# Kernel tuning notes

Hardware: AMD Instinct MI355X
Metric: run time of the kernel (lower is better)

The kernel has to match this reference:

```python
import jax, jax.numpy as jnp
import numpy as np

EPS = 1e-4


def setup_inputs() -> dict:
    key = jax.random.key(0)
    ks = jax.random.split(key, 16)
    N, D, H, K = 262144, 162, 256, 30
    s = 0.05  # weight init scale
    return {
        "Yh": jax.random.uniform(ks[0], (N, D), dtype=jnp.float32),
        "u": jax.random.uniform(ks[1], (1,), dtype=jnp.float32),
        "W1": jax.random.normal(ks[2], (D, H), dtype=jnp.float32) * s,
        "b1": jnp.zeros((H,), jnp.float32),
        "W2": jax.random.normal(ks[3], (H, H), dtype=jnp.float32) * s,
        "b2": jnp.zeros((H,), jnp.float32),
        "Wa": jax.random.normal(ks[4], (H, K), dtype=jnp.float32) * s,
        "ba": jnp.zeros((K,), jnp.float32),
        "Wb": jax.random.normal(ks[5], (H, K), dtype=jnp.float32) * s,
        "bb": jnp.zeros((K,), jnp.float32),
        "Wd1": jax.random.normal(ks[6], (K, H), dtype=jnp.float32) * s,
        "bd1": jnp.zeros((H,), jnp.float32),
        "Wd2": jax.random.normal(ks[7], (H, D), dtype=jnp.float32) * s,
        "bd2": jnp.zeros((D,), jnp.float32),
    }


def _stick_segments(v):
    # pi_k = v_k * prod_{j<k} (1 - v_j)  (vectorized exclusive cumprod,
    # replacing the original per-dim Python loop)
    cp = jnp.cumprod(1.0 - v, axis=1)  # [N, K]
    excl = jnp.concatenate([jnp.ones_like(v[:, :1]), cp[:, :-1]], axis=1)
    return v * excl


def reference(Yh, u, W1, b1, W2, b2, Wa, ba, Wb, bb, Wd1, bd1, Wd2, bd2):
    # encode_hsi: dense MLP -> positive Kumaraswamy params (softplus heads)
    h = jax.nn.relu(Yh @ W1 + b1)
    h = jax.nn.relu(h @ W2 + b2)
    alpha = jax.nn.softplus(h @ Wa + ba) + EPS  # param1_hsi [N, K]
    beta = jax.nn.softplus(h @ Wb + bb) + EPS   # param2_hsi [N, K]
    # Kumaraswamy reparametrization with a single shared uniform sample
    uu = u[0] * 0.98 + 0.01  # Uniform(0.01, 0.99) scalar
    v = (1.0 - uu ** (1.0 / beta)) ** (1.0 / alpha)  # [N, K]
    # set_v_K_to_one: force last stick proportion to 1
    v = jnp.concatenate([v[:, :-1], jnp.ones_like(v[:, :1])], axis=1)
    pi_h = _stick_segments(v)  # [N, K], rows sum to 1
    # decode: MLP -> sigmoid (positive outputs, recon.log() finite)
    d = jax.nn.relu(pi_h @ Wd1 + bd1)
    recon = jax.nn.sigmoid(d @ Wd2 + bd2)  # [N, D]
    return recon, alpha, beta, pi_h
```

## Files before the change

kernel.cpp:

```cpp
#include <hip/hip_runtime.h>
#include <hip/hip_bf16.h>

#define N_ROWS 262144
#define D_IN 162
#define H_DIM 256
#define K_DIM 30

using bf16_t = __hip_bfloat16;
typedef __attribute__((ext_vector_type(8))) short bf16x8;
typedef __attribute__((ext_vector_type(4))) float f32x4;

__device__ __forceinline__ int swz_idx(int row, int col) {
  int byte = (row << 9) + (col << 1);
  byte ^= (row & 7) << 4;
  return byte >> 1;
}

__device__ __forceinline__ float softplus_f(float x) {
  return (x > 15.f) ? x : log1pf(__expf(x));
}

__global__ void pack_b_kernel(const float* __restrict__ src, bf16_t* __restrict__ dst,
                              int K, int N, int Np, int KB) {
  int idx = blockIdx.x * 256 + threadIdx.x;
  int total = KB * Np * 32;
  if (idx >= total) return;
  int ks = idx & 31;
  int n  = (idx >> 5) % Np;
  int kb = idx / (32 * Np);
  int k  = kb * 32 + ks;
  float v = (k < K && n < N) ? src[k * N + n] : 0.f;
  dst[idx] = __float2bfloat16(v);
}

__global__ void pack_ab_kernel(const float* __restrict__ Wa, const float* __restrict__ Wb,
                               bf16_t* __restrict__ dst) {
  int idx = blockIdx.x * 256 + threadIdx.x;
  if (idx >= 8 * 64 * 32) return;
  int ks = idx & 31;
  int n  = (idx >> 5) & 63;
  int kb = idx >> 11;
  int k  = kb * 32 + ks;
  float v = 0.f;
  if (n < 30)                 v = Wa[k * 30 + n];
  else if (n >= 32 && n < 62) v = Wb[k * 30 + (n - 32)];
  dst[idx] = __float2bfloat16(v);
}

template<int KB, int NP>
__device__ __forceinline__ void gemm_tile(const bf16_t* __restrict__ A,
                                          const bf16_t* __restrict__ Bp,
                                          int colBase, int lr, int lg,
                                          f32x4 acc[4][4]) {
#pragma unroll
  for (int kb = 0; kb < KB; ++kb) {
    bf16x8 a[4], b[4];
#pragma unroll
    for (int m = 0; m < 4; ++m)
      a[m] = *reinterpret_cast<const bf16x8*>(A + swz_idx(16 * m + lr, kb * 32 + 8 * lg));
#pragma unroll
    for (int n = 0; n < 4; ++n)
      b[n] = *reinterpret_cast<const bf16x8*>(Bp + ((kb * NP + colBase + 16 * n + lr) << 5) + 8 * lg);
#pragma unroll
    for (int m = 0; m < 4; ++m)
#pragma unroll
      for (int n = 0; n < 4; ++n)
        acc[m][n] = __builtin_amdgcn_mfma_f32_16x16x32_bf16(a[m], b[n], acc[m][n], 0, 0, 0);
  }
}

__device__ __forceinline__ void epilogue_relu(f32x4 acc[4][4], const float* __restrict__ bias,
                                              bf16_t* __restrict__ Out, int colBase,
                                              int lr, int lg) {
#pragma unroll
  for (int n = 0; n < 4; ++n) {
    int col = colBase + 16 * n + lr;
    float bv = bias[col];
#pragma unroll
    for (int m = 0; m < 4; ++m)
#pragma unroll
      for (int i = 0; i < 4; ++i) {
        float x = acc[m][n][i] + bv;
        x = fmaxf(x, 0.f);
        Out[swz_idx(16 * m + 4 * lg + i, col)] = __float2bfloat16(x);
      }
  }
}

__launch_bounds__(256, 2)
__global__ void usdn_fused(const float* __restrict__ Yh, const float* __restrict__ u,
                           const float* __restrict__ b1, const float* __restrict__ b2,
                           const float* __restrict__ ba, const float* __restrict__ bb,
                           const float* __restrict__ bd1, const float* __restrict__ bd2,
                           const bf16_t* __restrict__ Wp1, const bf16_t* __restrict__ Wp2,
                           const bf16_t* __restrict__ Wpab, const bf16_t* __restrict__ Wpd1,
                           const bf16_t* __restrict__ Wpd2,
                           float* __restrict__ outRecon, float* __restrict__ outAlpha,
                           float* __restrict__ outBeta, float* __restrict__ outPi) {
  __shared__ bf16_t bufA[64 * 256];
  __shared__ bf16_t bufB[64 * 256];

  const int tid = threadIdx.x;
  const int w  = tid >> 6;
  const int l  = tid & 63;
  const int lr = l & 15;
  const int lg = l >> 4;
  const int r0 = blockIdx.x << 6;

  {
    const float4* src = reinterpret_cast<const float4*>(Yh + (size_t)r0 * D_IN);
    for (int i = tid; i < (64 * D_IN) / 4; i += 256) {
      float4 f = src[i];
      int base = i << 2;
#pragma unroll
      for (int e = 0; e < 4; ++e) {
        int idx = base + e;
        int row = idx / D_IN;
        int col = idx - row * D_IN;
        bufA[swz_idx(row, col)] = __float2bfloat16((&f.x)[e]);
      }
    }
    for (int i = tid; i < 64 * (192 - D_IN); i += 256) {
      int row = i / 30;
      int col = D_IN + (i - row * 30);
      bufA[swz_idx(row, col)] = __float2bfloat16(0.f);
    }
  }
  __syncthreads();

  {
    f32x4 acc[4][4] = {};
    gemm_tile<6, 256>(bufA, Wp1, w * 64, lr, lg, acc);
    epilogue_relu(acc, b1, bufB, w * 64, lr, lg);
  }
  __syncthreads();

  {
    f32x4 acc[4][4] = {};
    gemm_tile<8, 256>(bufB, Wp2, w * 64, lr, lg, acc);
    epilogue_relu(acc, b2, bufA, w * 64, lr, lg);
  }
  __syncthreads();

  {
    f32x4 acc3[4] = {};
#pragma unroll
    for (int kb = 0; kb < 8; ++kb) {
      bf16x8 a = *reinterpret_cast<const bf16x8*>(bufA + swz_idx(16 * w + lr, kb * 32 + 8 * lg));
#pragma unroll
      for (int n = 0; n < 4; ++n) {
        bf16x8 b = *reinterpret_cast<const bf16x8*>(Wpab + ((kb * 64 + 16 * n + lr) << 5) + 8 * lg);
        acc3[n] = __builtin_amdgcn_mfma_f32_16x16x32_bf16(a, b, acc3[n], 0, 0, 0);
      }
    }
    float uu  = u[0] * 0.98f + 0.01f;
    float l2u = log2f(uu);
    float* vbuf = reinterpret_cast<float*>(bufB);
#pragma unroll
    for (int n = 0; n < 2; ++n) {
      int j = 16 * n + lr;
      bool valid = (j < K_DIM);
      float bva = valid ? ba[j] : 0.f;
      float bvb = valid ? bb[j] : 0.f;
#pragma unroll
      for (int i = 0; i < 4; ++i) {
        int row = 16 * w + 4 * lg + i;
        if (valid) {
          float alpha = softplus_f(acc3[n][i] + bva) + 1e-4f;
          float beta  = softplus_f(acc3[n + 2][i] + bvb) + 1e-4f;
          size_t gro = (size_t)(r0 + row);
          outAlpha[gro * K_DIM + j] = alpha;
          outBeta [gro * K_DIM + j] = beta;
          float v;
          if (j == K_DIM - 1) v = 1.f;
          else {
            float t = exp2f(l2u / beta);
            v = exp2f(log2f(1.f - t) / alpha);
          }
          vbuf[row * 33 + j] = v;
        }
      }
    }
  }
  __syncthreads();

  if (tid < 64) {
    const float* vbuf = reinterpret_cast<const float*>(bufB);
    int row = tid;
    size_t gro = (size_t)(r0 + row);
    float ex = 1.f;
#pragma unroll
    for (int j = 0; j < K_DIM - 1; ++j) {
      float vj = vbuf[row * 33 + j];
      float pi = vj * ex;
      outPi[gro * K_DIM + j] = pi;
      bufA[row * 40 + j] = __float2bfloat16(pi);
      ex *= (1.f - vj);
    }
    outPi[gro * K_DIM + (K_DIM - 1)] = ex;
    bufA[row * 40 + 29] = __float2bfloat16(ex);
    bufA[row * 40 + 30] = __float2bfloat16(0.f);
    bufA[row * 40 + 31] = __float2bfloat16(0.f);
  }
  __syncthreads();

  {
    f32x4 acc[4][4] = {};
    bf16x8 a[4];
#pragma unroll
    for (int m = 0; m < 4; ++m)
      a[m] = *reinterpret_cast<const bf16x8*>(bufA + (16 * m + lr) * 40 + 8 * lg);
#pragma unroll
    for (int n = 0; n < 4; ++n) {
      bf16x8 b = *reinterpret_cast<const bf16x8*>(Wpd1 + ((w * 64 + 16 * n + lr) << 5) + 8 * lg);
#pragma unroll
      for (int m = 0; m < 4; ++m)
        acc[m][n] = __builtin_amdgcn_mfma_f32_16x16x32_bf16(a[m], b, acc[m][n], 0, 0, 0);
    }
    epilogue_relu(acc, bd1, bufB, w * 64, lr, lg);
  }
  __syncthreads();

  {
    f32x4 acc[4][3] = {};
#pragma unroll
    for (int kb = 0; kb < 8; ++kb) {
      bf16x8 a[4];
#pragma unroll
      for (int m = 0; m < 4; ++m)
        a[m] = *reinterpret_cast<const bf16x8*>(bufB + swz_idx(16 * m + lr, kb * 32 + 8 * lg));
#pragma unroll
      for (int n = 0; n < 3; ++n) {
        bf16x8 b = *reinterpret_cast<const bf16x8*>(Wpd2 + ((kb * 192 + w * 48 + 16 * n + lr) << 5) + 8 * lg);
#pragma unroll
        for (int m = 0; m < 4; ++m)
          acc[m][n] = __builtin_amdgcn_mfma_f32_16x16x32_bf16(a[m], b, acc[m][n], 0, 0, 0);
      }
    }
#pragma unroll
    for (int n = 0; n < 3; ++n) {
      int col = w * 48 + 16 * n + lr;
      if (col < D_IN) {
        float bv = bd2[col];
#pragma unroll
        for (int m = 0; m < 4; ++m)
#pragma unroll
          for (int i = 0; i < 4; ++i) {
            int row = 16 * m + 4 * lg + i;
            float x = acc[m][n][i] + bv;
            float s = 1.f / (1.f + __expf(-x));
            outRecon[(size_t)(r0 + row) * D_IN + col] = s;
          }
      }
    }
  }
}

extern "C" void kernel_launch(void* const* d_in, const int* in_sizes, int n_in,
                              void* d_out, int out_size, void* d_ws, size_t ws_size,
                              hipStream_t stream) {
  const float* Yh  = (const float*)d_in[0];
  const float* u   = (const float*)d_in[1];
  const float* W1  = (const float*)d_in[2];
  const float* b1  = (const float*)d_in[3];
  const float* W2  = (const float*)d_in[4];
  const float* b2  = (const float*)d_in[5];
  const float* Wa  = (const float*)d_in[6];
  const float* ba  = (const float*)d_in[7];
  const float* Wb  = (const float*)d_in[8];
  const float* bb  = (const float*)d_in[9];
  const float* Wd1 = (const float*)d_in[10];
  const float* bd1 = (const float*)d_in[11];
  const float* Wd2 = (const float*)d_in[12];
  const float* bd2 = (const float*)d_in[13];

  bf16_t* ws   = (bf16_t*)d_ws;
  bf16_t* Wp1  = ws;
  bf16_t* Wp2  = Wp1 + 49152;
  bf16_t* Wpab = Wp2 + 65536;
  bf16_t* Wpd1 = Wpab + 16384;
  bf16_t* Wpd2 = Wpd1 + 8192;

  float* outRecon = (float*)d_out;
  float* outAlpha = outRecon + (size_t)N_ROWS * D_IN;
  float* outBeta  = outAlpha + (size_t)N_ROWS * K_DIM;
  float* outPi    = outBeta  + (size_t)N_ROWS * K_DIM;

  pack_b_kernel<<<192, 256, 0, stream>>>(W1, Wp1, 162, 256, 256, 6);
  pack_b_kernel<<<256, 256, 0, stream>>>(W2, Wp2, 256, 256, 256, 8);
  pack_ab_kernel<<<64, 256, 0, stream>>>(Wa, Wb, Wpab);
  pack_b_kernel<<<32, 256, 0, stream>>>(Wd1, Wpd1, 30, 256, 256, 1);
  pack_b_kernel<<<192, 256, 0, stream>>>(Wd2, Wpd2, 256, 162, 192, 8);

  usdn_fused<<<N_ROWS / 64, 256, 0, stream>>>(Yh, u, b1, b2, ba, bb, bd1, bd2,
                                              Wp1, Wp2, Wpab, Wpd1, Wpd2,
                                              outRecon, outAlpha, outBeta, outPi);
}
```

Measured before the change: 308.5 us.

## Halve rows per block to 32 and raise occupancy to four blocks per CU

Each block now handles 32 rows instead of 64, which halves the LDS buffers (32 KB total) and the accumulator register tiles, and the launch bound goes from 2 to 4 blocks per CU. The second GEMM writes its output back into the same hidden buffer after an extra barrier, and the pi tile is placed inside the Y buffer, so the block needs only two shared buffers. The goal is more resident waves to hide global-memory and LDS latency. The cost is that every weight fragment is now read from global/L2 once per 32 rows instead of once per 64, which doubles weight traffic, and the alpha/beta stage runs on only two of the four waves.

```diff
diff --git a/kernel.cpp b/kernel.cpp
--- a/kernel.cpp
+++ b/kernel.cpp
@@ -5,6 +5,7 @@
 #define D_IN 162
 #define H_DIM 256
 #define K_DIM 30
+#define ROWS 32
 
 using bf16_t = __hip_bfloat16;
 typedef __attribute__((ext_vector_type(8))) short bf16x8;
@@ -47,47 +48,7 @@
   dst[idx] = __float2bfloat16(v);
 }
 
-template<int KB, int NP>
-__device__ __forceinline__ void gemm_tile(const bf16_t* __restrict__ A,
-                                          const bf16_t* __restrict__ Bp,
-                                          int colBase, int lr, int lg,
-                                          f32x4 acc[4][4]) {
-#pragma unroll
-  for (int kb = 0; kb < KB; ++kb) {
-    bf16x8 a[4], b[4];
-#pragma unroll
-    for (int m = 0; m < 4; ++m)
-      a[m] = *reinterpret_cast<const bf16x8*>(A + swz_idx(16 * m + lr, kb * 32 + 8 * lg));
-#pragma unroll
-    for (int n = 0; n < 4; ++n)
-      b[n] = *reinterpret_cast<const bf16x8*>(Bp + ((kb * NP + colBase + 16 * n + lr) << 5) + 8 * lg);
-#pragma unroll
-    for (int m = 0; m < 4; ++m)
-#pragma unroll
-      for (int n = 0; n < 4; ++n)
-        acc[m][n] = __builtin_amdgcn_mfma_f32_16x16x32_bf16(a[m], b[n], acc[m][n], 0, 0, 0);
-  }
-}
-
-__device__ __forceinline__ void epilogue_relu(f32x4 acc[4][4], const float* __restrict__ bias,
-                                              bf16_t* __restrict__ Out, int colBase,
-                                              int lr, int lg) {
-#pragma unroll
-  for (int n = 0; n < 4; ++n) {
-    int col = colBase + 16 * n + lr;
-    float bv = bias[col];
-#pragma unroll
-    for (int m = 0; m < 4; ++m)
-#pragma unroll
-      for (int i = 0; i < 4; ++i) {
-        float x = acc[m][n][i] + bv;
-        x = fmaxf(x, 0.f);
-        Out[swz_idx(16 * m + 4 * lg + i, col)] = __float2bfloat16(x);
-      }
-  }
-}
-
-__launch_bounds__(256, 2)
+__launch_bounds__(256, 4)
 __global__ void usdn_fused(const float* __restrict__ Yh, const float* __restrict__ u,
                            const float* __restrict__ b1, const float* __restrict__ b2,
                            const float* __restrict__ ba, const float* __restrict__ bb,
@@ -97,56 +58,111 @@
                            const bf16_t* __restrict__ Wpd2,
                            float* __restrict__ outRecon, float* __restrict__ outAlpha,
                            float* __restrict__ outBeta, float* __restrict__ outPi) {
-  __shared__ bf16_t bufA[64 * 256];
-  __shared__ bf16_t bufB[64 * 256];
+  __shared__ bf16_t bufY[ROWS * 256];
+  __shared__ bf16_t bufH[ROWS * 256];
 
   const int tid = threadIdx.x;
   const int w  = tid >> 6;
   const int l  = tid & 63;
   const int lr = l & 15;
   const int lg = l >> 4;
-  const int r0 = blockIdx.x << 6;
+  const int r0 = blockIdx.x * ROWS;
 
   {
     const float4* src = reinterpret_cast<const float4*>(Yh + (size_t)r0 * D_IN);
-    for (int i = tid; i < (64 * D_IN) / 4; i += 256) {
-      float4 f = src[i];
-      int base = i << 2;
-#pragma unroll
-      for (int e = 0; e < 4; ++e) {
-        int idx = base + e;
-        int row = idx / D_IN;
-        int col = idx - row * D_IN;
-        bufA[swz_idx(row, col)] = __float2bfloat16((&f.x)[e]);
-      }
-    }
-    for (int i = tid; i < 64 * (192 - D_IN); i += 256) {
+#pragma unroll
+    for (int it = 0; it < 6; ++it) {
+      int i = tid + it * 256;
+      if (i < (ROWS * D_IN) / 4) {
+        float4 f = src[i];
+        int base = i << 2;
+#pragma unroll
+        for (int e = 0; e < 4; ++e) {
+          int idx = base + e;
+          int row = idx / D_IN;
+          int col = idx - row * D_IN;
+          bufY[swz_idx(row, col)] = __float2bfloat16((&f.x)[e]);
+        }
+      }
+    }
+    for (int i = tid; i < ROWS * 30; i += 256) {
       int row = i / 30;
       int col = D_IN + (i - row * 30);
-      bufA[swz_idx(row, col)] = __float2bfloat16(0.f);
-    }
-  }
-  __syncthreads();
-
-  {
-    f32x4 acc[4][4] = {};
-    gemm_tile<6, 256>(bufA, Wp1, w * 64, lr, lg, acc);
-    epilogue_relu(acc, b1, bufB, w * 64, lr, lg);
-  }
-  __syncthreads();
-
-  {
-    f32x4 acc[4][4] = {};
-    gemm_tile<8, 256>(bufB, Wp2, w * 64, lr, lg, acc);
-    epilogue_relu(acc, b2, bufA, w * 64, lr, lg);
-  }
-  __syncthreads();
-
-  {
+      bufY[swz_idx(row, col)] = __float2bfloat16(0.f);
+    }
+  }
+  __syncthreads();
+
+  {
+    f32x4 acc[2][4] = {};
+#pragma unroll
+    for (int kb = 0; kb < 6; ++kb) {
+      bf16x8 a[2], b[4];
+#pragma unroll
+      for (int m = 0; m < 2; ++m)
+        a[m] = *reinterpret_cast<const bf16x8*>(bufY + swz_idx(16 * m + lr, kb * 32 + 8 * lg));
+#pragma unroll
+      for (int n = 0; n < 4; ++n)
+        b[n] = *reinterpret_cast<const bf16x8*>(Wp1 + ((kb * 256 + w * 64 + 16 * n + lr) << 5) + 8 * lg);
+#pragma unroll
+      for (int m = 0; m < 2; ++m)
+#pragma unroll
+        for (int n = 0; n < 4; ++n)
+          acc[m][n] = __builtin_amdgcn_mfma_f32_16x16x32_bf16(a[m], b[n], acc[m][n], 0, 0, 0);
+    }
+#pragma unroll
+    for (int n = 0; n < 4; ++n) {
+      int col = w * 64 + 16 * n + lr;
+      float bv = b1[col];
+#pragma unroll
+      for (int m = 0; m < 2; ++m)
+#pragma unroll
+        for (int i = 0; i < 4; ++i) {
+          float x = fmaxf(acc[m][n][i] + bv, 0.f);
+          bufH[swz_idx(16 * m + 4 * lg + i, col)] = __float2bfloat16(x);
+        }
+    }
+  }
+  __syncthreads();
+
+  {
+    f32x4 acc[2][4] = {};
+#pragma unroll
+    for (int kb = 0; kb < 8; ++kb) {
+      bf16x8 a[2], b[4];
+#pragma unroll
+      for (int m = 0; m < 2; ++m)
+        a[m] = *reinterpret_cast<const bf16x8*>(bufH + swz_idx(16 * m + lr, kb * 32 + 8 * lg));
+#pragma unroll
+      for (int n = 0; n < 4; ++n)
+        b[n] = *reinterpret_cast<const bf16x8*>(Wp2 + ((kb * 256 + w * 64 + 16 * n + lr) << 5) + 8 * lg);
+#pragma unroll
+      for (int m = 0; m < 2; ++m)
+#pragma unroll
+        for (int n = 0; n < 4; ++n)
+          acc[m][n] = __builtin_amdgcn_mfma_f32_16x16x32_bf16(a[m], b[n], acc[m][n], 0, 0, 0);
+    }
+    __syncthreads();
+#pragma unroll
+    for (int n = 0; n < 4; ++n) {
+      int col = w * 64 + 16 * n + lr;
+      float bv = b2[col];
+#pragma unroll
+      for (int m = 0; m < 2; ++m)
+#pragma unroll
+        for (int i = 0; i < 4; ++i) {
+          float x = fmaxf(acc[m][n][i] + bv, 0.f);
+          bufH[swz_idx(16 * m + 4 * lg + i, col)] = __float2bfloat16(x);
+        }
+    }
+  }
+  __syncthreads();
+
+  if (w < 2) {
     f32x4 acc3[4] = {};
 #pragma unroll
     for (int kb = 0; kb < 8; ++kb) {
-      bf16x8 a = *reinterpret_cast<const bf16x8*>(bufA + swz_idx(16 * w + lr, kb * 32 + 8 * lg));
+      bf16x8 a = *reinterpret_cast<const bf16x8*>(bufH + swz_idx(16 * w + lr, kb * 32 + 8 * lg));
 #pragma unroll
       for (int n = 0; n < 4; ++n) {
         bf16x8 b = *reinterpret_cast<const bf16x8*>(Wpab + ((kb * 64 + 16 * n + lr) << 5) + 8 * lg);
@@ -155,7 +171,7 @@
     }
     float uu  = u[0] * 0.98f + 0.01f;
     float l2u = log2f(uu);
-    float* vbuf = reinterpret_cast<float*>(bufB);
+    float* vbuf = reinterpret_cast<float*>(bufY);
 #pragma unroll
     for (int n = 0; n < 2; ++n) {
       int j = 16 * n + lr;
@@ -184,56 +200,71 @@
   }
   __syncthreads();
 
-  if (tid < 64) {
-    const float* vbuf = reinterpret_cast<const float*>(bufB);
-    int row = tid;
-    size_t gro = (size_t)(r0 + row);
-    float ex = 1.f;
-#pragma unroll
-    for (int j = 0; j < K_DIM - 1; ++j) {
-      float vj = vbuf[row * 33 + j];
-      float pi = vj * ex;
-      outPi[gro * K_DIM + j] = pi;
-      bufA[row * 40 + j] = __float2bfloat16(pi);
-      ex *= (1.f - vj);
-    }
-    outPi[gro * K_DIM + (K_DIM - 1)] = ex;
-    bufA[row * 40 + 29] = __float2bfloat16(ex);
-    bufA[row * 40 + 30] = __float2bfloat16(0.f);
-    bufA[row * 40 + 31] = __float2bfloat16(0.f);
-  }
-  __syncthreads();
-
-  {
-    f32x4 acc[4][4] = {};
-    bf16x8 a[4];
-#pragma unroll
-    for (int m = 0; m < 4; ++m)
-      a[m] = *reinterpret_cast<const bf16x8*>(bufA + (16 * m + lr) * 40 + 8 * lg);
+  {
+    bf16_t* piT = bufY + 4096;
+    if (tid < ROWS) {
+      const float* vbuf = reinterpret_cast<const float*>(bufY);
+      int row = tid;
+      size_t gro = (size_t)(r0 + row);
+      float ex = 1.f;
+#pragma unroll
+      for (int j = 0; j < K_DIM - 1; ++j) {
+        float vj = vbuf[row * 33 + j];
+        float pi = vj * ex;
+        outPi[gro * K_DIM + j] = pi;
+        piT[row * 40 + j] = __float2bfloat16(pi);
+        ex *= (1.f - vj);
+      }
+      outPi[gro * K_DIM + (K_DIM - 1)] = ex;
+      piT[row * 40 + 29] = __float2bfloat16(ex);
+      piT[row * 40 + 30] = __float2bfloat16(0.f);
+      piT[row * 40 + 31] = __float2bfloat16(0.f);
+    }
+  }
+  __syncthreads();
+
+  {
+    const bf16_t* piT = bufY + 4096;
+    f32x4 acc[2][4] = {};
+    bf16x8 a[2];
+#pragma unroll
+    for (int m = 0; m < 2; ++m)
+      a[m] = *reinterpret_cast<const bf16x8*>(piT + (16 * m + lr) * 40 + 8 * lg);
 #pragma unroll
     for (int n = 0; n < 4; ++n) {
       bf16x8 b = *reinterpret_cast<const bf16x8*>(Wpd1 + ((w * 64 + 16 * n + lr) << 5) + 8 * lg);
 #pragma unroll
-      for (int m = 0; m < 4; ++m)
+      for (int m = 0; m < 2; ++m)
         acc[m][n] = __builtin_amdgcn_mfma_f32_16x16x32_bf16(a[m], b, acc[m][n], 0, 0, 0);
     }
-    epilogue_relu(acc, bd1, bufB, w * 64, lr, lg);
-  }
-  __syncthreads();
-
-  {
-    f32x4 acc[4][3] = {};
+#pragma unroll
+    for (int n = 0; n < 4; ++n) {
+      int col = w * 64 + 16 * n + lr;
+      float bv = bd1[col];
+#pragma unroll
+      for (int m = 0; m < 2; ++m)
+#pragma unroll
+        for (int i = 0; i < 4; ++i) {
+          float x = fmaxf(acc[m][n][i] + bv, 0.f);
+          bufH[swz_idx(16 * m + 4 * lg + i, col)] = __float2bfloat16(x);
+        }
+    }
+  }
+  __syncthreads();
+
+  {
+    f32x4 acc[2][3] = {};
 #pragma unroll
     for (int kb = 0; kb < 8; ++kb) {
-      bf16x8 a[4];
-#pragma unroll
-      for (int m = 0; m < 4; ++m)
-        a[m] = *reinterpret_cast<const bf16x8*>(bufB + swz_idx(16 * m + lr, kb * 32 + 8 * lg));
+      bf16x8 a[2];
+#pragma unroll
+      for (int m = 0; m < 2; ++m)
+        a[m] = *reinterpret_cast<const bf16x8*>(bufH + swz_idx(16 * m + lr, kb * 32 + 8 * lg));
 #pragma unroll
       for (int n = 0; n < 3; ++n) {
         bf16x8 b = *reinterpret_cast<const bf16x8*>(Wpd2 + ((kb * 192 + w * 48 + 16 * n + lr) << 5) + 8 * lg);
 #pragma unroll
-        for (int m = 0; m < 4; ++m)
+        for (int m = 0; m < 2; ++m)
           acc[m][n] = __builtin_amdgcn_mfma_f32_16x16x32_bf16(a[m], b, acc[m][n], 0, 0, 0);
       }
     }
@@ -243,7 +274,7 @@
       if (col < D_IN) {
         float bv = bd2[col];
 #pragma unroll
-        for (int m = 0; m < 4; ++m)
+        for (int m = 0; m < 2; ++m)
 #pragma unroll
           for (int i = 0; i < 4; ++i) {
             int row = 16 * m + 4 * lg + i;
@@ -292,7 +323,7 @@
   pack_b_kernel<<<32, 256, 0, stream>>>(Wd1, Wpd1, 30, 256, 256, 1);
   pack_b_kernel<<<192, 256, 0, stream>>>(Wd2, Wpd2, 256, 162, 192, 8);
 
-  usdn_fused<<<N_ROWS / 64, 256, 0, stream>>>(Yh, u, b1, b2, ba, bb, bd1, bd2,
-                                              Wp1, Wp2, Wpab, Wpd1, Wpd2,
-                                              outRecon, outAlpha, outBeta, outPi);
-}
+  usdn_fused<<<N_ROWS / ROWS, 256, 0, stream>>>(Yh, u, b1, b2, ba, bb, bd1, bd2,
+                                                Wp1, Wp2, Wpab, Wpd1, Wpd2,
+                                                outRecon, outAlpha, outBeta, outPi);
+}
```

Measured after the change: 322.2 us. 1.04x slower.

## Halve rows per block, swap MFMA operands, and use a single LDS buffer

Applied to the files above, without the earlier changes.

Each block now handles 32 rows instead of 64, and all stages share one 32 KB LDS buffer, with launch bounds raised to target four blocks per CU. The GEMMs are reformulated with weights as the A operand and activations as B, which transposes the accumulator layout. That allows packed bf16x4 epilogue stores, accumulators seeded with the bias, and interleaved alpha/beta columns. Output stores for recon, alpha, beta and pi are vectorised as float2. Pi is now written out from its bf16-rounded LDS copy, which lowers its precision, and halving the rows per block doubles how often each block reloads the weights.

```diff
diff --git a/kernel.cpp b/kernel.cpp
--- a/kernel.cpp
+++ b/kernel.cpp
@@ -3,19 +3,30 @@
 
 #define N_ROWS 262144
 #define D_IN 162
-#define H_DIM 256
 #define K_DIM 30
+#define ROWS 32
 
 using bf16_t = __hip_bfloat16;
 typedef __attribute__((ext_vector_type(8))) short bf16x8;
 typedef __attribute__((ext_vector_type(4))) float f32x4;
 
-__device__ __forceinline__ int swz_idx(int row, int col) {
-  int byte = (row << 9) + (col << 1);
-  byte ^= (row & 7) << 4;
-  return byte >> 1;
-}
-
+__device__ __forceinline__ int swz_byte(int row, int col) {
+  int b = (row << 9) + (col << 1);
+  return b ^ ((row & 7) << 4);
+}
+
+__device__ __forceinline__ uint32_t bf16b(float x) {
+  return (uint32_t)__builtin_bit_cast(unsigned short, __float2bfloat16(x));
+}
+__device__ __forceinline__ uint32_t pack2(float lo, float hi) {
+  return bf16b(lo) | (bf16b(hi) << 16);
+}
+__device__ __forceinline__ float unpk_lo(uint32_t p) {
+  return __bfloat162float(__builtin_bit_cast(__hip_bfloat16, (unsigned short)(p & 0xffff)));
+}
+__device__ __forceinline__ float unpk_hi(uint32_t p) {
+  return __bfloat162float(__builtin_bit_cast(__hip_bfloat16, (unsigned short)(p >> 16)));
+}
 __device__ __forceinline__ float softplus_f(float x) {
   return (x > 15.f) ? x : log1pf(__expf(x));
 }
@@ -41,53 +52,72 @@
   int n  = (idx >> 5) & 63;
   int kb = idx >> 11;
   int k  = kb * 32 + ks;
-  float v = 0.f;
-  if (n < 30)                 v = Wa[k * 30 + n];
-  else if (n >= 32 && n < 62) v = Wb[k * 30 + (n - 32)];
+  int j = n >> 1, s = n & 1;
+  float v = (j < K_DIM) ? (s ? Wb[k * K_DIM + j] : Wa[k * K_DIM + j]) : 0.f;
   dst[idx] = __float2bfloat16(v);
 }
 
-template<int KB, int NP>
-__device__ __forceinline__ void gemm_tile(const bf16_t* __restrict__ A,
-                                          const bf16_t* __restrict__ Bp,
-                                          int colBase, int lr, int lg,
-                                          f32x4 acc[4][4]) {
+template<int KB, int NP, int NMO>
+__device__ __forceinline__ void gemm_acc(const uint8_t* lds, int srcOff,
+                                         const bf16_t* __restrict__ Wp, int ocBase,
+                                         int lr, int lg, f32x4 (&acc)[NMO][2]) {
+  int bE[2], bO[2];
+#pragma unroll
+  for (int nr = 0; nr < 2; ++nr) {
+    bE[nr] = srcOff + swz_byte(16 * nr + lr, 8 * lg);
+    bO[nr] = srcOff + swz_byte(16 * nr + lr, 32 + 8 * lg);
+  }
 #pragma unroll
   for (int kb = 0; kb < KB; ++kb) {
-    bf16x8 a[4], b[4];
-#pragma unroll
-    for (int m = 0; m < 4; ++m)
-      a[m] = *reinterpret_cast<const bf16x8*>(A + swz_idx(16 * m + lr, kb * 32 + 8 * lg));
-#pragma unroll
-    for (int n = 0; n < 4; ++n)
-      b[n] = *reinterpret_cast<const bf16x8*>(Bp + ((kb * NP + colBase + 16 * n + lr) << 5) + 8 * lg);
-#pragma unroll
-    for (int m = 0; m < 4; ++m)
-#pragma unroll
-      for (int n = 0; n < 4; ++n)
-        acc[m][n] = __builtin_amdgcn_mfma_f32_16x16x32_bf16(a[m], b[n], acc[m][n], 0, 0, 0);
-  }
-}
-
-__device__ __forceinline__ void epilogue_relu(f32x4 acc[4][4], const float* __restrict__ bias,
-                                              bf16_t* __restrict__ Out, int colBase,
-                                              int lr, int lg) {
-#pragma unroll
-  for (int n = 0; n < 4; ++n) {
-    int col = colBase + 16 * n + lr;
-    float bv = bias[col];
-#pragma unroll
-    for (int m = 0; m < 4; ++m)
-#pragma unroll
-      for (int i = 0; i < 4; ++i) {
-        float x = acc[m][n][i] + bv;
-        x = fmaxf(x, 0.f);
-        Out[swz_idx(16 * m + 4 * lg + i, col)] = __float2bfloat16(x);
-      }
-  }
-}
-
-__launch_bounds__(256, 2)
+    bf16x8 wf[NMO];
+#pragma unroll
+    for (int mo = 0; mo < NMO; ++mo)
+      wf[mo] = *reinterpret_cast<const bf16x8*>(Wp + ((kb * NP + ocBase + 16 * mo + lr) << 5) + 8 * lg);
+    bf16x8 hf[2];
+#pragma unroll
+    for (int nr = 0; nr < 2; ++nr) {
+      int base = (kb & 1) ? bO[nr] : bE[nr];
+      hf[nr] = *reinterpret_cast<const bf16x8*>(lds + base + (kb >> 1) * 128);
+    }
+#pragma unroll
+    for (int mo = 0; mo < NMO; ++mo)
+#pragma unroll
+      for (int nr = 0; nr < 2; ++nr)
+        acc[mo][nr] = __builtin_amdgcn_mfma_f32_16x16x32_bf16(wf[mo], hf[nr], acc[mo][nr], 0, 0, 0);
+  }
+}
+
+template<int NMO>
+__device__ __forceinline__ void acc_bias_init(const float* __restrict__ bias, int ocBase,
+                                              int lg, f32x4 (&acc)[NMO][2]) {
+#pragma unroll
+  for (int mo = 0; mo < NMO; ++mo) {
+    float4 bv = *reinterpret_cast<const float4*>(bias + ocBase + 16 * mo + 4 * lg);
+    f32x4 t = {bv.x, bv.y, bv.z, bv.w};
+#pragma unroll
+    for (int nr = 0; nr < 2; ++nr) acc[mo][nr] = t;
+  }
+}
+
+template<int NMO>
+__device__ __forceinline__ void epi_relu_store(uint8_t* lds, int dstOff, int ocBase,
+                                               int lr, int lg, f32x4 (&acc)[NMO][2]) {
+#pragma unroll
+  for (int mo = 0; mo < NMO; ++mo)
+#pragma unroll
+    for (int nr = 0; nr < 2; ++nr) {
+      int row = 16 * nr + lr;
+      int col = ocBase + 16 * mo + 4 * lg;
+      float x0 = fmaxf(acc[mo][nr][0], 0.f), x1 = fmaxf(acc[mo][nr][1], 0.f);
+      float x2 = fmaxf(acc[mo][nr][2], 0.f), x3 = fmaxf(acc[mo][nr][3], 0.f);
+      uint2 p; p.x = pack2(x0, x1); p.y = pack2(x2, x3);
+      *reinterpret_cast<uint2*>(lds + dstOff + swz_byte(row, col)) = p;
+    }
+}
+
+#define OFF_H 16384
+#define OFF_PI 8192
+__launch_bounds__(256, 4)
 __global__ void usdn_fused(const float* __restrict__ Yh, const float* __restrict__ u,
                            const float* __restrict__ b1, const float* __restrict__ b2,
                            const float* __restrict__ ba, const float* __restrict__ bb,
@@ -97,160 +127,164 @@
                            const bf16_t* __restrict__ Wpd2,
                            float* __restrict__ outRecon, float* __restrict__ outAlpha,
                            float* __restrict__ outBeta, float* __restrict__ outPi) {
-  __shared__ bf16_t bufA[64 * 256];
-  __shared__ bf16_t bufB[64 * 256];
+  __shared__ __align__(16) uint8_t lds[32768];
 
   const int tid = threadIdx.x;
   const int w  = tid >> 6;
   const int l  = tid & 63;
   const int lr = l & 15;
   const int lg = l >> 4;
-  const int r0 = blockIdx.x << 6;
-
-  {
-    const float4* src = reinterpret_cast<const float4*>(Yh + (size_t)r0 * D_IN);
-    for (int i = tid; i < (64 * D_IN) / 4; i += 256) {
-      float4 f = src[i];
-      int base = i << 2;
-#pragma unroll
-      for (int e = 0; e < 4; ++e) {
-        int idx = base + e;
-        int row = idx / D_IN;
-        int col = idx - row * D_IN;
-        bufA[swz_idx(row, col)] = __float2bfloat16((&f.x)[e]);
-      }
-    }
-    for (int i = tid; i < 64 * (192 - D_IN); i += 256) {
-      int row = i / 30;
-      int col = D_IN + (i - row * 30);
-      bufA[swz_idx(row, col)] = __float2bfloat16(0.f);
-    }
-  }
-  __syncthreads();
-
-  {
-    f32x4 acc[4][4] = {};
-    gemm_tile<6, 256>(bufA, Wp1, w * 64, lr, lg, acc);
-    epilogue_relu(acc, b1, bufB, w * 64, lr, lg);
-  }
-  __syncthreads();
-
-  {
-    f32x4 acc[4][4] = {};
-    gemm_tile<8, 256>(bufB, Wp2, w * 64, lr, lg, acc);
-    epilogue_relu(acc, b2, bufA, w * 64, lr, lg);
-  }
-  __syncthreads();
-
-  {
-    f32x4 acc3[4] = {};
-#pragma unroll
-    for (int kb = 0; kb < 8; ++kb) {
-      bf16x8 a = *reinterpret_cast<const bf16x8*>(bufA + swz_idx(16 * w + lr, kb * 32 + 8 * lg));
-#pragma unroll
-      for (int n = 0; n < 4; ++n) {
-        bf16x8 b = *reinterpret_cast<const bf16x8*>(Wpab + ((kb * 64 + 16 * n + lr) << 5) + 8 * lg);
-        acc3[n] = __builtin_amdgcn_mfma_f32_16x16x32_bf16(a, b, acc3[n], 0, 0, 0);
-      }
-    }
+  const int r0 = blockIdx.x * ROWS;
+
+  {
+    int row = tid >> 3, l8 = tid & 7;
+    const float2* src = reinterpret_cast<const float2*>(Yh + (size_t)(r0 + row) * D_IN);
+#pragma unroll
+    for (int it = 0; it < 12; ++it) {
+      int f2 = l8 + it * 8;
+      uint32_t p = 0;
+      if (f2 < 81) { float2 v = src[f2]; p = pack2(v.x, v.y); }
+      if (f2 < 96) *reinterpret_cast<uint32_t*>(lds + swz_byte(row, f2 * 2)) = p;
+    }
+  }
+  __syncthreads();
+
+  {
+    f32x4 acc[4][2];
+    acc_bias_init<4>(b1, w * 64, lg, acc);
+    gemm_acc<6, 256, 4>(lds, 0, Wp1, w * 64, lr, lg, acc);
+    epi_relu_store<4>(lds, OFF_H, w * 64, lr, lg, acc);
+  }
+  __syncthreads();
+
+  {
+    f32x4 acc[4][2];
+    acc_bias_init<4>(b2, w * 64, lg, acc);
+    gemm_acc<8, 256, 4>(lds, OFF_H, Wp2, w * 64, lr, lg, acc);
+    __syncthreads();
+    epi_relu_store<4>(lds, OFF_H, w * 64, lr, lg, acc);
+  }
+  __syncthreads();
+
+  float regA0[2], regA1[2], regB0[2], regB1[2];
+  int   j0 = 8 * w + 2 * lg;
+  {
+    bool jv = (j0 < K_DIM);
+    float ba0 = jv ? ba[j0] : 0.f,     bb0 = jv ? bb[j0] : 0.f;
+    float ba1 = jv ? ba[j0 + 1] : 0.f, bb1 = jv ? bb[j0 + 1] : 0.f;
+    f32x4 acc[1][2];
+    f32x4 binit = {ba0, bb0, ba1, bb1};
+    acc[0][0] = binit; acc[0][1] = binit;
+    gemm_acc<8, 64, 1>(lds, OFF_H, Wpab, 16 * w, lr, lg, acc);
+
     float uu  = u[0] * 0.98f + 0.01f;
     float l2u = log2f(uu);
-    float* vbuf = reinterpret_cast<float*>(bufB);
-#pragma unroll
-    for (int n = 0; n < 2; ++n) {
-      int j = 16 * n + lr;
-      bool valid = (j < K_DIM);
-      float bva = valid ? ba[j] : 0.f;
-      float bvb = valid ? bb[j] : 0.f;
-#pragma unroll
-      for (int i = 0; i < 4; ++i) {
-        int row = 16 * w + 4 * lg + i;
-        if (valid) {
-          float alpha = softplus_f(acc3[n][i] + bva) + 1e-4f;
-          float beta  = softplus_f(acc3[n + 2][i] + bvb) + 1e-4f;
-          size_t gro = (size_t)(r0 + row);
-          outAlpha[gro * K_DIM + j] = alpha;
-          outBeta [gro * K_DIM + j] = beta;
-          float v;
-          if (j == K_DIM - 1) v = 1.f;
-          else {
-            float t = exp2f(l2u / beta);
-            v = exp2f(log2f(1.f - t) / alpha);
-          }
-          vbuf[row * 33 + j] = v;
+    float* vbuf = reinterpret_cast<float*>(lds);
+#pragma unroll
+    for (int nr = 0; nr < 2; ++nr) {
+      int row = 16 * nr + lr;
+      float a0 = softplus_f(acc[0][nr][0]) + 1e-4f;
+      float b0v = softplus_f(acc[0][nr][1]) + 1e-4f;
+      float a1 = softplus_f(acc[0][nr][2]) + 1e-4f;
+      float b1v = softplus_f(acc[0][nr][3]) + 1e-4f;
+      regA0[nr] = a0; regB0[nr] = b0v; regA1[nr] = a1; regB1[nr] = b1v;
+      if (jv) {
+        if (j0 < K_DIM - 1) {
+          float t = exp2f(l2u / b0v);
+          vbuf[row * 33 + j0] = exp2f(log2f(1.f - t) / a0);
+        }
+        if (j0 + 1 < K_DIM - 1) {
+          float t = exp2f(l2u / b1v);
+          vbuf[row * 33 + j0 + 1] = exp2f(log2f(1.f - t) / a1);
         }
       }
     }
   }
   __syncthreads();
 
-  if (tid < 64) {
-    const float* vbuf = reinterpret_cast<const float*>(bufB);
+  if (tid < ROWS) {
+    const float* vbuf = reinterpret_cast<const float*>(lds);
+    bf16_t* piT = reinterpret_cast<bf16_t*>(lds + OFF_PI);
     int row = tid;
-    size_t gro = (size_t)(r0 + row);
     float ex = 1.f;
 #pragma unroll
     for (int j = 0; j < K_DIM - 1; ++j) {
       float vj = vbuf[row * 33 + j];
       float pi = vj * ex;
-      outPi[gro * K_DIM + j] = pi;
-      bufA[row * 40 + j] = __float2bfloat16(pi);
+      piT[row * 40 + j] = __float2bfloat16(pi);
       ex *= (1.f - vj);
     }
-    outPi[gro * K_DIM + (K_DIM - 1)] = ex;
-    bufA[row * 40 + 29] = __float2bfloat16(ex);
-    bufA[row * 40 + 30] = __float2bfloat16(0.f);
-    bufA[row * 40 + 31] = __float2bfloat16(0.f);
-  }
-  __syncthreads();
-
-  {
-    f32x4 acc[4][4] = {};
-    bf16x8 a[4];
-#pragma unroll
-    for (int m = 0; m < 4; ++m)
-      a[m] = *reinterpret_cast<const bf16x8*>(bufA + (16 * m + lr) * 40 + 8 * lg);
-#pragma unroll
-    for (int n = 0; n < 4; ++n) {
-      bf16x8 b = *reinterpret_cast<const bf16x8*>(Wpd1 + ((w * 64 + 16 * n + lr) << 5) + 8 * lg);
-#pragma unroll
-      for (int m = 0; m < 4; ++m)
-        acc[m][n] = __builtin_amdgcn_mfma_f32_16x16x32_bf16(a[m], b, acc[m][n], 0, 0, 0);
-    }
-    epilogue_relu(acc, bd1, bufB, w * 64, lr, lg);
-  }
-  __syncthreads();
-
-  {
-    f32x4 acc[4][3] = {};
-#pragma unroll
-    for (int kb = 0; kb < 8; ++kb) {
-      bf16x8 a[4];
-#pragma unroll
-      for (int m = 0; m < 4; ++m)
-        a[m] = *reinterpret_cast<const bf16x8*>(bufB + swz_idx(16 * m + lr, kb * 32 + 8 * lg));
-#pragma unroll
-      for (int n = 0; n < 3; ++n) {
-        bf16x8 b = *reinterpret_cast<const bf16x8*>(Wpd2 + ((kb * 192 + w * 48 + 16 * n + lr) << 5) + 8 * lg);
-#pragma unroll
-        for (int m = 0; m < 4; ++m)
-          acc[m][n] = __builtin_amdgcn_mfma_f32_16x16x32_bf16(a[m], b, acc[m][n], 0, 0, 0);
+    piT[row * 40 + (K_DIM - 1)] = __float2bfloat16(ex);
+    piT[row * 40 + 30] = __float2bfloat16(0.f);
+    piT[row * 40 + 31] = __float2bfloat16(0.f);
+  }
+  __syncthreads();
+
+  {
+    f32x4 acc[4][2];
+    acc_bias_init<4>(bd1, w * 64, lg, acc);
+    bf16x8 pf[2];
+#pragma unroll
+    for (int nr = 0; nr < 2; ++nr)
+      pf[nr] = *reinterpret_cast<const bf16x8*>(lds + OFF_PI + (16 * nr + lr) * 80 + 16 * lg);
+#pragma unroll
+    for (int mo = 0; mo < 4; ++mo) {
+      bf16x8 wf = *reinterpret_cast<const bf16x8*>(Wpd1 + ((w * 64 + 16 * mo + lr) << 5) + 8 * lg);
+#pragma unroll
+      for (int nr = 0; nr < 2; ++nr)
+        acc[mo][nr] = __builtin_amdgcn_mfma_f32_16x16x32_bf16(wf, pf[nr], acc[mo][nr], 0, 0, 0);
+    }
+    epi_relu_store<4>(lds, OFF_H, w * 64, lr, lg, acc);
+  }
+  __syncthreads();
+
+  {
+    f32x4 acc[3][2];
+#pragma unroll
+    for (int mo = 0; mo < 3; ++mo) {
+      int col0 = 48 * w + 16 * mo + 4 * lg;
+      f32x4 t;
+#pragma unroll
+      for (int i = 0; i < 4; ++i) t[i] = (col0 + i < D_IN) ? bd2[col0 + i] : 0.f;
+#pragma unroll
+      for (int nr = 0; nr < 2; ++nr) acc[mo][nr] = t;
+    }
+    gemm_acc<8, 192, 3>(lds, OFF_H, Wpd2, 48 * w, lr, lg, acc);
+#pragma unroll
+    for (int mo = 0; mo < 3; ++mo) {
+      int col0 = 48 * w + 16 * mo + 4 * lg;
+#pragma unroll
+      for (int nr = 0; nr < 2; ++nr) {
+        int row = 16 * nr + lr;
+        float s0 = 1.f / (1.f + __expf(-acc[mo][nr][0]));
+        float s1 = 1.f / (1.f + __expf(-acc[mo][nr][1]));
+        float s2 = 1.f / (1.f + __expf(-acc[mo][nr][2]));
+        float s3 = 1.f / (1.f + __expf(-acc[mo][nr][3]));
+        float* dst = outRecon + (size_t)(r0 + row) * D_IN + col0;
+        if (col0 < D_IN)     *reinterpret_cast<float2*>(dst)     = make_float2(s0, s1);
+        if (col0 + 2 < D_IN) *reinterpret_cast<float2*>(dst + 2) = make_float2(s2, s3);
       }
     }
-#pragma unroll
-    for (int n = 0; n < 3; ++n) {
-      int col = w * 48 + 16 * n + lr;
-      if (col < D_IN) {
-        float bv = bd2[col];
-#pragma unroll
-        for (int m = 0; m < 4; ++m)
-#pragma unroll
-          for (int i = 0; i < 4; ++i) {
-            int row = 16 * m + 4 * lg + i;
-            float x = acc[m][n][i] + bv;
-            float s = 1.f / (1.f + __expf(-x));
-            outRecon[(size_t)(r0 + row) * D_IN + col] = s;
-          }
+  }
+
+  if (j0 < K_DIM) {
+#pragma unroll
+    for (int nr = 0; nr < 2; ++nr) {
+      int row = 16 * nr + lr;
+      size_t base = (size_t)(r0 + row) * K_DIM + j0;
+      *reinterpret_cast<float2*>(outAlpha + base) = make_float2(regA0[nr], regA1[nr]);
+      *reinterpret_cast<float2*>(outBeta  + base) = make_float2(regB0[nr], regB1[nr]);
+    }
+  }
+  {
+    int row = tid >> 3, l8 = tid & 7;
+#pragma unroll
+    for (int half = 0; half < 2; ++half) {
+      int f2 = l8 + half * 8;
+      if (f2 < 15) {
+        uint32_t pp = *reinterpret_cast<const uint32_t*>(lds + OFF_PI + row * 80 + f2 * 4);
+        *reinterpret_cast<float2*>(outPi + (size_t)(r0 + row) * K_DIM + f2 * 2) =
+            make_float2(unpk_lo(pp), unpk_hi(pp));
       }
     }
   }
@@ -292,7 +326,7 @@
   pack_b_kernel<<<32, 256, 0, stream>>>(Wd1, Wpd1, 30, 256, 256, 1);
   pack_b_kernel<<<192, 256, 0, stream>>>(Wd2, Wpd2, 256, 162, 192, 8);
 
-  usdn_fused<<<N_ROWS / 64, 256, 0, stream>>>(Yh, u, b1, b2, ba, bb, bd1, bd2,
-                                              Wp1, Wp2, Wpab, Wpd1, Wpd2,
-                                              outRecon, outAlpha, outBeta, outPi);
-}
+  usdn_fused<<<N_ROWS / ROWS, 256, 0, stream>>>(Yh, u, b1, b2, ba, bb, bd1, bd2,
+                                                Wp1, Wp2, Wpab, Wpd1, Wpd2,
+                                                outRecon, outAlpha, outBeta, outPi);
+}
```

Result: faster. 280.7 us (-9.0%).
